# Performance work log

Hardware: AMD Instinct MI355X
Metric: run time of the kernel (lower is better)

## Reference

```python
import jax, jax.numpy as jnp
import numpy as np

H = 128
NUM_IN = 384
B, N, K = 4, 2048, 48
SCALE = 30.0
EPS = 1e-5


def _layernorm(x, gamma, beta):
    mu = jnp.mean(x, axis=-1, keepdims=True)
    var = jnp.mean(jnp.square(x - mu), axis=-1, keepdims=True)
    return (x - mu) * jax.lax.rsqrt(var + EPS) * gamma + beta


def setup_inputs() -> dict:
    key = jax.random.key(0)
    ks = jax.random.split(key, 12)
    s = lambda fan_in: 1.0 / np.sqrt(fan_in)
    inp = {
        "h_V": jax.random.normal(ks[0], (B, N, H), jnp.float32),
        "h_E": jax.random.normal(ks[1], (B, N, K, NUM_IN), jnp.float32),
        "mask_V": jnp.ones((B, N), jnp.float32),
        "mask_attend": jnp.ones((B, N, K), jnp.float32),
        # message MLP
        "W1": jax.random.uniform(ks[2], (H + NUM_IN, H), jnp.float32, -s(H + NUM_IN), s(H + NUM_IN)),
        "b1": jnp.zeros((H,), jnp.float32),
        "W2": jax.random.uniform(ks[3], (H, H), jnp.float32, -s(H), s(H)),
        "b2": jnp.zeros((H,), jnp.float32),
        "W3": jax.random.uniform(ks[4], (H, H), jnp.float32, -s(H), s(H)),
        "b3": jnp.zeros((H,), jnp.float32),
        # layernorms
        "g1": jnp.ones((H,), jnp.float32), "be1": jnp.zeros((H,), jnp.float32),
        "g2": jnp.ones((H,), jnp.float32), "be2": jnp.zeros((H,), jnp.float32),
        # FFN
        "Wi": jax.random.uniform(ks[5], (H, 4 * H), jnp.float32, -s(H), s(H)),
        "bi": jnp.zeros((4 * H,), jnp.float32),
        "Wo": jax.random.uniform(ks[6], (4 * H, H), jnp.float32, -s(4 * H), s(4 * H)),
        "bo": jnp.zeros((H,), jnp.float32),
        # rezero alpha (init 0.01)
        "alpha": jnp.array([0.01], jnp.float32),
    }
    return inp


def reference(h_V, h_E, mask_V, mask_attend, W1, b1, W2, b2, W3, b3,
              g1, be1, g2, be2, Wi, bi, Wo, bo, alpha):
    gelu = lambda x: jax.nn.gelu(x, approximate=False)
    # broadcast-concat node features onto each neighbor edge: [B,N,K,H+num_in]
    h_V_expand = jnp.broadcast_to(h_V[:, :, None, :], (*h_E.shape[:-1], h_V.shape[-1]))
    h_EV = jnp.concatenate([h_V_expand, h_E], axis=-1)
    # 3-layer message MLP
    h_message = gelu(jnp.einsum("bnkf,fh->bnkh", h_EV, W1) + b1)
    h_message = gelu(jnp.einsum("bnkh,hg->bnkg", h_message, W2) + b2)
    h_message = jnp.einsum("bnkg,gh->bnkh", h_message, W3) + b3
    h_message = mask_attend[..., None] * h_message
    # masked sum-reduce over neighbors
    dh = jnp.sum(h_message, axis=-2) / SCALE
    # residual (rezero) + LayerNorm  (dropout = identity in eval)
    h = _layernorm(alpha * dh + h_V, g1, be1)
    # position-wise FFN
    dh = gelu(h @ Wi + bi) @ Wo + bo
    h = _layernorm(alpha * dh + h, g2, be2)
    # node mask
    h = mask_V[..., None] * h
    return h
```

## Files before the change

kernel.cpp:

```cpp
#include <hip/hip_runtime.h>

#define LN_EPS 1e-5f
#define RSCALE (1.0f / 30.0f)

typedef short short8  __attribute__((ext_vector_type(8)));
typedef short short4v __attribute__((ext_vector_type(4)));
typedef float f32x4   __attribute__((ext_vector_type(4)));

__device__ __forceinline__ unsigned short f2bf(float f) {
    unsigned u = __builtin_bit_cast(unsigned, f);
    u = u + 0x7FFFu + ((u >> 16) & 1u);
    return (unsigned short)(u >> 16);
}

__device__ __forceinline__ float gelu_f(float x) {
    float u  = 0.7978845608028654f * (x + 0.044715f * x * x * x);
    float e  = __expf(-2.0f * fabsf(u));
    float t  = 1.0f - 2.0f * e / (1.0f + e);
    return 0.5f * x * (1.0f + copysignf(t, u));
}

__device__ __forceinline__ f32x4 zero4() {
    f32x4 v; v.x = 0.f; v.y = 0.f; v.z = 0.f; v.w = 0.f; return v;
}

__global__ __launch_bounds__(256) void prep_w(
    const float* __restrict__ W1, const float* __restrict__ W2,
    const float* __restrict__ W3,
    unsigned short* __restrict__ w1t, unsigned short* __restrict__ w2t,
    unsigned short* __restrict__ w3t)
{
    int t = blockIdx.x * 256 + threadIdx.x;
    if (t < 65536) {
        int m = t & 127, k = t >> 7;
        w1t[m * 512 + k] = f2bf(W1[k * 128 + m]);
    } else if (t < 81920) {
        int u = t - 65536, m = u & 127, k = u >> 7;
        w2t[m * 128 + k] = f2bf(W2[k * 128 + m]);
    } else if (t < 98304) {
        int u = t - 81920, m = u & 127, k = u >> 7;
        w3t[m * 128 + k] = f2bf(W3[k * 128 + m]);
    }
}

__global__ __launch_bounds__(256, 2) void edge_mlp(
    const float* __restrict__ hV, const float* __restrict__ hE,
    const float* __restrict__ mAtt,
    const unsigned short* __restrict__ w1t, const unsigned short* __restrict__ w2t,
    const unsigned short* __restrict__ w3t,
    const float* __restrict__ b1, const float* __restrict__ b2,
    const float* __restrict__ b3, float* __restrict__ dh)
{
    __shared__ short A1[96 * 64];
    __shared__ short Wb[128 * 64];
    __shared__ short Hb[2][96 * 128];
    __shared__ float mb[96];

    const int tid  = threadIdx.x;
    const int lane = tid & 63;
    const int wv   = tid >> 6;
    const int g    = wv & 1;
    const int mh   = wv >> 1;
    const int ln   = lane & 15;
    const int kg   = lane >> 4;
    const int node0 = blockIdx.x * 2;

    if (tid < 96) mb[tid] = mAtt[node0 * 48 + tid];

    f32x4 acc[4][3];
#pragma unroll
    for (int j = 0; j < 4; ++j)
#pragma unroll
        for (int i = 0; i < 3; ++i) acc[j][i] = zero4();

    const int srow = tid >> 4;
    const int c4   = (tid & 15) * 4;
    const int kb_w = c4 >> 3;
    const int c4lo = c4 & 4;

    for (int c = 0; c < 8; ++c) {
        const int kc = c * 64;
        if (kc < 128) {
#pragma unroll
            for (int rep = 0; rep < 6; ++rep) {
                const int r = rep * 16 + srow;
                const float4 v = *(const float4*)(hV + (node0 + (r >= 48 ? 1 : 0)) * 128 + kc + c4);
                short4v p;
                p.x = (short)f2bf(v.x); p.y = (short)f2bf(v.y);
                p.z = (short)f2bf(v.z); p.w = (short)f2bf(v.w);
                *(short4v*)&A1[r * 64 + ((kb_w ^ (r & 7)) * 8) + c4lo] = p;
            }
        } else {
#pragma unroll
            for (int rep = 0; rep < 6; ++rep) {
                const int r = rep * 16 + srow;
                const float4 v = *(const float4*)(hE + (node0 * 48 + r) * 384 + (kc - 128) + c4);
                short4v p;
                p.x = (short)f2bf(v.x); p.y = (short)f2bf(v.y);
                p.z = (short)f2bf(v.z); p.w = (short)f2bf(v.w);
                *(short4v*)&A1[r * 64 + ((kb_w ^ (r & 7)) * 8) + c4lo] = p;
            }
        }
#pragma unroll
        for (int rep = 0; rep < 4; ++rep) {
            const int u = rep * 256 + tid;
            const int m = u >> 3, kb = u & 7;
            short8 val = *(const short8*)(w1t + m * 512 + kc + kb * 8);
            *(short8*)&Wb[m * 64 + ((kb ^ (m & 7)) * 8)] = val;
        }
        __syncthreads();
#pragma unroll
        for (int s = 0; s < 2; ++s) {
            const int kb = s * 4 + kg;
            short8 bf[3], af[4];
#pragma unroll
            for (int i = 0; i < 3; ++i) {
                const int r = (3 * g + i) * 16 + ln;
                bf[i] = *(const short8*)&A1[r * 64 + ((kb ^ (r & 7)) * 8)];
            }
#pragma unroll
            for (int j = 0; j < 4; ++j) {
                const int m = (4 * mh + j) * 16 + ln;
                af[j] = *(const short8*)&Wb[m * 64 + ((kb ^ (m & 7)) * 8)];
            }
#pragma unroll
            for (int j = 0; j < 4; ++j)
#pragma unroll
                for (int i = 0; i < 3; ++i)
                    acc[j][i] = __builtin_amdgcn_mfma_f32_16x16x32_bf16(af[j], bf[i], acc[j][i], 0, 0, 0);
        }
        __syncthreads();
    }

#pragma unroll
    for (int j = 0; j < 4; ++j) {
        const int m0 = (4 * mh + j) * 16 + kg * 4;
        const float4 bb = *(const float4*)(b1 + m0);
#pragma unroll
        for (int i = 0; i < 3; ++i) {
            const int r = (3 * g + i) * 16 + ln;
            short4v p;
            p.x = (short)f2bf(gelu_f(acc[j][i].x + bb.x));
            p.y = (short)f2bf(gelu_f(acc[j][i].y + bb.y));
            p.z = (short)f2bf(gelu_f(acc[j][i].z + bb.z));
            p.w = (short)f2bf(gelu_f(acc[j][i].w + bb.w));
            *(short4v*)&Hb[0][r * 128 + (((m0 >> 3) ^ (r & 7)) * 8) + (m0 & 4)] = p;
        }
    }

    for (int L = 0; L < 2; ++L) {
#pragma unroll
        for (int j = 0; j < 4; ++j)
#pragma unroll
            for (int i = 0; i < 3; ++i) acc[j][i] = zero4();

        const unsigned short* wt = (L == 0) ? w2t : w3t;
        for (int c = 0; c < 2; ++c) {
            const int kc = c * 64;
#pragma unroll
            for (int rep = 0; rep < 4; ++rep) {
                const int u = rep * 256 + tid;
                const int m = u >> 3, kb = u & 7;
                short8 val = *(const short8*)(wt + m * 128 + kc + kb * 8);
                *(short8*)&Wb[m * 64 + ((kb ^ (m & 7)) * 8)] = val;
            }
            __syncthreads();
#pragma unroll
            for (int s = 0; s < 2; ++s) {
                const int kbW = s * 4 + kg;
                const int kbH = c * 8 + s * 4 + kg;
                short8 bf[3], af[4];
#pragma unroll
                for (int i = 0; i < 3; ++i) {
                    const int r = (3 * g + i) * 16 + ln;
                    bf[i] = *(const short8*)&Hb[L][r * 128 + ((kbH ^ (r & 7)) * 8)];
                }
#pragma unroll
                for (int j = 0; j < 4; ++j) {
                    const int m = (4 * mh + j) * 16 + ln;
                    af[j] = *(const short8*)&Wb[m * 64 + ((kbW ^ (m & 7)) * 8)];
                }
#pragma unroll
                for (int j = 0; j < 4; ++j)
#pragma unroll
                    for (int i = 0; i < 3; ++i)
                        acc[j][i] = __builtin_amdgcn_mfma_f32_16x16x32_bf16(af[j], bf[i], acc[j][i], 0, 0, 0);
            }
            __syncthreads();
        }

        if (L == 0) {
#pragma unroll
            for (int j = 0; j < 4; ++j) {
                const int m0 = (4 * mh + j) * 16 + kg * 4;
                const float4 bb = *(const float4*)(b2 + m0);
#pragma unroll
                for (int i = 0; i < 3; ++i) {
                    const int r = (3 * g + i) * 16 + ln;
                    short4v p;
                    p.x = (short)f2bf(gelu_f(acc[j][i].x + bb.x));
                    p.y = (short)f2bf(gelu_f(acc[j][i].y + bb.y));
                    p.z = (short)f2bf(gelu_f(acc[j][i].z + bb.z));
                    p.w = (short)f2bf(gelu_f(acc[j][i].w + bb.w));
                    *(short4v*)&Hb[1][r * 128 + (((m0 >> 3) ^ (r & 7)) * 8) + (m0 & 4)] = p;
                }
            }
        } else {
#pragma unroll
            for (int j = 0; j < 4; ++j) {
                const int m0 = (4 * mh + j) * 16 + kg * 4;
                const float4 bb = *(const float4*)(b3 + m0);
                float s0 = 0.f, s1 = 0.f, s2 = 0.f, s3 = 0.f;
#pragma unroll
                for (int i = 0; i < 3; ++i) {
                    const int r = (3 * g + i) * 16 + ln;
                    const float mk = mb[r];
                    s0 += (acc[j][i].x + bb.x) * mk;
                    s1 += (acc[j][i].y + bb.y) * mk;
                    s2 += (acc[j][i].z + bb.z) * mk;
                    s3 += (acc[j][i].w + bb.w) * mk;
                }
#pragma unroll
                for (int off = 1; off < 16; off <<= 1) {
                    s0 += __shfl_xor(s0, off, 64);
                    s1 += __shfl_xor(s1, off, 64);
                    s2 += __shfl_xor(s2, off, 64);
                    s3 += __shfl_xor(s3, off, 64);
                }
                if (ln == 0) {
                    float4 o;
                    o.x = s0 * RSCALE; o.y = s1 * RSCALE;
                    o.z = s2 * RSCALE; o.w = s3 * RSCALE;
                    *(float4*)&dh[(node0 + g) * 128 + m0] = o;
                }
            }
        }
    }
}

__global__ __launch_bounds__(256, 2) void node_ffn(
    const float* __restrict__ hV, const float* __restrict__ dh,
    const float* __restrict__ maskV,
    const float* __restrict__ g1, const float* __restrict__ be1,
    const float* __restrict__ g2, const float* __restrict__ be2,
    const float* __restrict__ Wi, const float* __restrict__ bi,
    const float* __restrict__ Wo, const float* __restrict__ bo,
    const float* __restrict__ alphap, float* __restrict__ out)
{
    __shared__ float hbuf[16 * 132];
    __shared__ float hidb[16 * 516];
    __shared__ float obuf[16 * 132];

    const int tid = threadIdx.x;
    const float al = alphap[0];
    const int nb = blockIdx.x * 16;

    {
        const int m = tid >> 4, s = tid & 15;
        const int i0 = s * 8;
        const int base = (nb + m) * 128 + i0;
        float x[8];
        {
            float4 a0 = *(const float4*)(dh + base);
            float4 a1 = *(const float4*)(dh + base + 4);
            float4 v0 = *(const float4*)(hV + base);
            float4 v1 = *(const float4*)(hV + base + 4);
            x[0] = v0.x + al * a0.x; x[1] = v0.y + al * a0.y;
            x[2] = v0.z + al * a0.z; x[3] = v0.w + al * a0.w;
            x[4] = v1.x + al * a1.x; x[5] = v1.y + al * a1.y;
            x[6] = v1.z + al * a1.z; x[7] = v1.w + al * a1.w;
        }
        float sm = 0.f;
#pragma unroll
        for (int q = 0; q < 8; ++q) sm += x[q];
#pragma unroll
        for (int off = 1; off < 16; off <<= 1) sm += __shfl_xor(sm, off, 64);
        const float mu = sm * (1.0f / 128.0f);
        float vs = 0.f;
#pragma unroll
        for (int q = 0; q < 8; ++q) { float d = x[q] - mu; vs += d * d; }
#pragma unroll
        for (int off = 1; off < 16; off <<= 1) vs += __shfl_xor(vs, off, 64);
        const float rs = rsqrtf(vs * (1.0f / 128.0f) + LN_EPS);
#pragma unroll
        for (int q = 0; q < 8; ++q)
            hbuf[m * 132 + i0 + q] = (x[q] - mu) * rs * g1[i0 + q] + be1[i0 + q];
    }
    __syncthreads();

    {
        const int jg = tid & 127, mhh = tid >> 7;
        const int j4 = jg * 4;
        float acc[8][4];
#pragma unroll
        for (int mm = 0; mm < 8; ++mm)
#pragma unroll
            for (int jj = 0; jj < 4; ++jj) acc[mm][jj] = 0.f;
        for (int i0 = 0; i0 < 128; i0 += 4) {
            float4 w0 = *(const float4*)(Wi + (i0 + 0) * 512 + j4);
            float4 w1 = *(const float4*)(Wi + (i0 + 1) * 512 + j4);
            float4 w2 = *(const float4*)(Wi + (i0 + 2) * 512 + j4);
            float4 w3 = *(const float4*)(Wi + (i0 + 3) * 512 + j4);
#pragma unroll
            for (int mm = 0; mm < 8; ++mm) {
                float4 h4 = *(const float4*)&hbuf[(mhh * 8 + mm) * 132 + i0];
                acc[mm][0] += h4.x * w0.x + h4.y * w1.x + h4.z * w2.x + h4.w * w3.x;
                acc[mm][1] += h4.x * w0.y + h4.y * w1.y + h4.z * w2.y + h4.w * w3.y;
                acc[mm][2] += h4.x * w0.z + h4.y * w1.z + h4.z * w2.z + h4.w * w3.z;
                acc[mm][3] += h4.x * w0.w + h4.y * w1.w + h4.z * w2.w + h4.w * w3.w;
            }
        }
        float4 bb = *(const float4*)(bi + j4);
#pragma unroll
        for (int mm = 0; mm < 8; ++mm) {
            float4 o;
            o.x = gelu_f(acc[mm][0] + bb.x);
            o.y = gelu_f(acc[mm][1] + bb.y);
            o.z = gelu_f(acc[mm][2] + bb.z);
            o.w = gelu_f(acc[mm][3] + bb.w);
            *(float4*)&hidb[(mhh * 8 + mm) * 516 + j4] = o;
        }
    }
    __syncthreads();

    {
        const int m = tid >> 4;
        const int n8 = (tid & 15) * 8;
        float4 r0, r1;
        r0.x = r0.y = r0.z = r0.w = 0.f;
        r1.x = r1.y = r1.z = r1.w = 0.f;
        for (int j0 = 0; j0 < 512; j0 += 4) {
            float4 hh = *(const float4*)&hidb[m * 516 + j0];
            float hq[4] = {hh.x, hh.y, hh.z, hh.w};
#pragma unroll
            for (int jj = 0; jj < 4; ++jj) {
                float4 w0 = *(const float4*)(Wo + (j0 + jj) * 128 + n8);
                float4 w1 = *(const float4*)(Wo + (j0 + jj) * 128 + n8 + 4);
                r0.x += hq[jj] * w0.x; r0.y += hq[jj] * w0.y;
                r0.z += hq[jj] * w0.z; r0.w += hq[jj] * w0.w;
                r1.x += hq[jj] * w1.x; r1.y += hq[jj] * w1.y;
                r1.z += hq[jj] * w1.z; r1.w += hq[jj] * w1.w;
            }
        }
        float4 q0 = *(const float4*)(bo + n8);
        float4 q1 = *(const float4*)(bo + n8 + 4);
        r0.x += q0.x; r0.y += q0.y; r0.z += q0.z; r0.w += q0.w;
        r1.x += q1.x; r1.y += q1.y; r1.z += q1.z; r1.w += q1.w;
        *(float4*)&obuf[m * 132 + n8]     = r0;
        *(float4*)&obuf[m * 132 + n8 + 4] = r1;
    }
    __syncthreads();

    {
        const int m = tid >> 4, s = tid & 15;
        const int i0 = s * 8;
        float x[8];
#pragma unroll
        for (int q = 0; q < 8; ++q)
            x[q] = hbuf[m * 132 + i0 + q] + al * obuf[m * 132 + i0 + q];
        float sm = 0.f;
#pragma unroll
        for (int q = 0; q < 8; ++q) sm += x[q];
#pragma unroll
        for (int off = 1; off < 16; off <<= 1) sm += __shfl_xor(sm, off, 64);
        const float mu = sm * (1.0f / 128.0f);
        float vs = 0.f;
#pragma unroll
        for (int q = 0; q < 8; ++q) { float d = x[q] - mu; vs += d * d; }
#pragma unroll
        for (int off = 1; off < 16; off <<= 1) vs += __shfl_xor(vs, off, 64);
        const float rs = rsqrtf(vs * (1.0f / 128.0f) + LN_EPS);
        const float mk = maskV[nb + m];
        float y[8];
#pragma unroll
        for (int q = 0; q < 8; ++q)
            y[q] = ((x[q] - mu) * rs * g2[i0 + q] + be2[i0 + q]) * mk;
        float4 o0, o1;
        o0.x = y[0]; o0.y = y[1]; o0.z = y[2]; o0.w = y[3];
        o1.x = y[4]; o1.y = y[5]; o1.z = y[6]; o1.w = y[7];
        const int base = (nb + m) * 128 + i0;
        *(float4*)(out + base)     = o0;
        *(float4*)(out + base + 4) = o1;
    }
}

extern "C" void kernel_launch(void* const* d_in, const int* in_sizes, int n_in,
                              void* d_out, int out_size, void* d_ws, size_t ws_size,
                              hipStream_t stream)
{
    const float* hV  = (const float*)d_in[0];
    const float* hE  = (const float*)d_in[1];
    const float* mV  = (const float*)d_in[2];
    const float* mA  = (const float*)d_in[3];
    const float* W1  = (const float*)d_in[4];
    const float* b1  = (const float*)d_in[5];
    const float* W2  = (const float*)d_in[6];
    const float* b2  = (const float*)d_in[7];
    const float* W3  = (const float*)d_in[8];
    const float* b3  = (const float*)d_in[9];
    const float* g1  = (const float*)d_in[10];
    const float* be1 = (const float*)d_in[11];
    const float* g2  = (const float*)d_in[12];
    const float* be2 = (const float*)d_in[13];
    const float* Wi  = (const float*)d_in[14];
    const float* bi  = (const float*)d_in[15];
    const float* Wo  = (const float*)d_in[16];
    const float* bo  = (const float*)d_in[17];
    const float* al  = (const float*)d_in[18];
    float* out = (float*)d_out;

    float* dh = (float*)d_ws;
    unsigned short* w1t = (unsigned short*)((char*)d_ws + (size_t)4194304);
    unsigned short* w2t = w1t + 65536;
    unsigned short* w3t = w2t + 16384;

    prep_w  <<<384,  256, 0, stream>>>(W1, W2, W3, w1t, w2t, w3t);
    edge_mlp<<<4096, 256, 0, stream>>>(hV, hE, mA, w1t, w2t, w3t, b1, b2, b3, dh);
    node_ffn<<<512,  256, 0, stream>>>(hV, dh, mV, g1, be1, g2, be2, Wi, bi, Wo, bo, al, out);
}
```

Baseline: 989.0 us.

## Precompute per-node h_V projection once and drop node K-chunks from edge GEMM

The node part of the first layer (h_V · W1[:128]) is the same for all 48 neighbours, so it is now computed once per node in fp32 and used to seed the MFMA accumulators, together with b1. The edge GEMM's K loop shrinks from 8 chunks to 6. This cuts redundant MFMA work and repeated h_V loads and conversions. The second hidden buffer is dropped so LDS use falls, and launch bounds rise to 3 blocks per CU for more occupancy. The cost is a small scalar fp32 dot product per block that reads W1 columns with stride, though these should stay in cache.

```diff
diff --git a/kernel.cpp b/kernel.cpp
--- a/kernel.cpp
+++ b/kernel.cpp
@@ -27,33 +27,34 @@
 __global__ __launch_bounds__(256) void prep_w(
     const float* __restrict__ W1, const float* __restrict__ W2,
     const float* __restrict__ W3,
-    unsigned short* __restrict__ w1t, unsigned short* __restrict__ w2t,
+    unsigned short* __restrict__ w1bt, unsigned short* __restrict__ w2t,
     unsigned short* __restrict__ w3t)
 {
     int t = blockIdx.x * 256 + threadIdx.x;
-    if (t < 65536) {
-        int m = t & 127, k = t >> 7;
-        w1t[m * 512 + k] = f2bf(W1[k * 128 + m]);
+    if (t < 49152) {
+        int m = t & 127, kk = t >> 7;
+        w1bt[m * 384 + kk] = f2bf(W1[(kk + 128) * 128 + m]);
+    } else if (t < 65536) {
+        int u = t - 49152, m = u & 127, k = u >> 7;
+        w2t[m * 128 + k] = f2bf(W2[k * 128 + m]);
     } else if (t < 81920) {
         int u = t - 65536, m = u & 127, k = u >> 7;
-        w2t[m * 128 + k] = f2bf(W2[k * 128 + m]);
-    } else if (t < 98304) {
-        int u = t - 81920, m = u & 127, k = u >> 7;
         w3t[m * 128 + k] = f2bf(W3[k * 128 + m]);
     }
 }
 
-__global__ __launch_bounds__(256, 2) void edge_mlp(
+__global__ __launch_bounds__(256, 3) void edge_mlp(
     const float* __restrict__ hV, const float* __restrict__ hE,
     const float* __restrict__ mAtt,
-    const unsigned short* __restrict__ w1t, const unsigned short* __restrict__ w2t,
+    const float* __restrict__ W1, const float* __restrict__ b1,
+    const unsigned short* __restrict__ w1bt, const unsigned short* __restrict__ w2t,
     const unsigned short* __restrict__ w3t,
-    const float* __restrict__ b1, const float* __restrict__ b2,
-    const float* __restrict__ b3, float* __restrict__ dh)
+    const float* __restrict__ b2, const float* __restrict__ b3,
+    float* __restrict__ dh)
 {
-    __shared__ short A1[96 * 64];
-    __shared__ short Wb[128 * 64];
-    __shared__ short Hb[2][96 * 128];
+    __shared__ __align__(16) short A1[96 * 64];
+    __shared__ __align__(16) short Wb[128 * 64];
+    __shared__ __align__(16) short Hb[96 * 128];
     __shared__ float mb[96];
 
     const int tid  = threadIdx.x;
@@ -65,47 +66,58 @@
     const int kg   = lane >> 4;
     const int node0 = blockIdx.x * 2;
 
-    if (tid < 96) mb[tid] = mAtt[node0 * 48 + tid];
-
-    f32x4 acc[4][3];
-#pragma unroll
-    for (int j = 0; j < 4; ++j)
-#pragma unroll
-        for (int i = 0; i < 3; ++i) acc[j][i] = zero4();
-
     const int srow = tid >> 4;
     const int c4   = (tid & 15) * 4;
     const int kb_w = c4 >> 3;
     const int c4lo = c4 & 4;
 
-    for (int c = 0; c < 8; ++c) {
+    if (tid < 96) mb[tid] = mAtt[node0 * 48 + tid];
+
+    float* nv = (float*)A1;
+    {
+        const int gg = tid >> 7, m = tid & 127;
+        const float* hv = hV + (node0 + gg) * 128;
+        const float* wc = W1 + m;
+        float a0 = 0.f, a1 = 0.f, a2 = 0.f, a3 = 0.f;
+        for (int k = 0; k < 128; k += 4) {
+            const float4 h4 = *(const float4*)(hv + k);
+            a0 += h4.x * wc[(k + 0) * 128];
+            a1 += h4.y * wc[(k + 1) * 128];
+            a2 += h4.z * wc[(k + 2) * 128];
+            a3 += h4.w * wc[(k + 3) * 128];
+        }
+        nv[tid] = b1[m] + (a0 + a1) + (a2 + a3);
+    }
+    __syncthreads();
+
+    f32x4 acc[4][3];
+#pragma unroll
+    for (int j = 0; j < 4; ++j) {
+        const float4 iv = *(const float4*)&nv[g * 128 + (4 * mh + j) * 16 + kg * 4];
+#pragma unroll
+        for (int i = 0; i < 3; ++i) {
+            acc[j][i].x = iv.x; acc[j][i].y = iv.y;
+            acc[j][i].z = iv.z; acc[j][i].w = iv.w;
+        }
+    }
+    __syncthreads();
+
+    for (int c = 0; c < 6; ++c) {
         const int kc = c * 64;
-        if (kc < 128) {
-#pragma unroll
-            for (int rep = 0; rep < 6; ++rep) {
-                const int r = rep * 16 + srow;
-                const float4 v = *(const float4*)(hV + (node0 + (r >= 48 ? 1 : 0)) * 128 + kc + c4);
-                short4v p;
-                p.x = (short)f2bf(v.x); p.y = (short)f2bf(v.y);
-                p.z = (short)f2bf(v.z); p.w = (short)f2bf(v.w);
-                *(short4v*)&A1[r * 64 + ((kb_w ^ (r & 7)) * 8) + c4lo] = p;
-            }
-        } else {
-#pragma unroll
-            for (int rep = 0; rep < 6; ++rep) {
-                const int r = rep * 16 + srow;
-                const float4 v = *(const float4*)(hE + (node0 * 48 + r) * 384 + (kc - 128) + c4);
-                short4v p;
-                p.x = (short)f2bf(v.x); p.y = (short)f2bf(v.y);
-                p.z = (short)f2bf(v.z); p.w = (short)f2bf(v.w);
-                *(short4v*)&A1[r * 64 + ((kb_w ^ (r & 7)) * 8) + c4lo] = p;
-            }
+#pragma unroll
+        for (int rep = 0; rep < 6; ++rep) {
+            const int r = rep * 16 + srow;
+            const float4 v = *(const float4*)(hE + (node0 * 48 + r) * 384 + kc + c4);
+            short4v p;
+            p.x = (short)f2bf(v.x); p.y = (short)f2bf(v.y);
+            p.z = (short)f2bf(v.z); p.w = (short)f2bf(v.w);
+            *(short4v*)&A1[r * 64 + ((kb_w ^ (r & 7)) * 8) + c4lo] = p;
         }
 #pragma unroll
         for (int rep = 0; rep < 4; ++rep) {
             const int u = rep * 256 + tid;
             const int m = u >> 3, kb = u & 7;
-            short8 val = *(const short8*)(w1t + m * 512 + kc + kb * 8);
+            short8 val = *(const short8*)(w1bt + m * 384 + kc + kb * 8);
             *(short8*)&Wb[m * 64 + ((kb ^ (m & 7)) * 8)] = val;
         }
         __syncthreads();
@@ -135,16 +147,15 @@
 #pragma unroll
     for (int j = 0; j < 4; ++j) {
         const int m0 = (4 * mh + j) * 16 + kg * 4;
-        const float4 bb = *(const float4*)(b1 + m0);
 #pragma unroll
         for (int i = 0; i < 3; ++i) {
             const int r = (3 * g + i) * 16 + ln;
             short4v p;
-            p.x = (short)f2bf(gelu_f(acc[j][i].x + bb.x));
-            p.y = (short)f2bf(gelu_f(acc[j][i].y + bb.y));
-            p.z = (short)f2bf(gelu_f(acc[j][i].z + bb.z));
-            p.w = (short)f2bf(gelu_f(acc[j][i].w + bb.w));
-            *(short4v*)&Hb[0][r * 128 + (((m0 >> 3) ^ (r & 7)) * 8) + (m0 & 4)] = p;
+            p.x = (short)f2bf(gelu_f(acc[j][i].x));
+            p.y = (short)f2bf(gelu_f(acc[j][i].y));
+            p.z = (short)f2bf(gelu_f(acc[j][i].z));
+            p.w = (short)f2bf(gelu_f(acc[j][i].w));
+            *(short4v*)&Hb[r * 128 + (((m0 >> 3) ^ (r & 7)) * 8) + (m0 & 4)] = p;
         }
     }
 
@@ -173,7 +184,7 @@
 #pragma unroll
                 for (int i = 0; i < 3; ++i) {
                     const int r = (3 * g + i) * 16 + ln;
-                    bf[i] = *(const short8*)&Hb[L][r * 128 + ((kbH ^ (r & 7)) * 8)];
+                    bf[i] = *(const short8*)&Hb[r * 128 + ((kbH ^ (r & 7)) * 8)];
                 }
 #pragma unroll
                 for (int j = 0; j < 4; ++j) {
@@ -202,7 +213,7 @@
                     p.y = (short)f2bf(gelu_f(acc[j][i].y + bb.y));
                     p.z = (short)f2bf(gelu_f(acc[j][i].z + bb.z));
                     p.w = (short)f2bf(gelu_f(acc[j][i].w + bb.w));
-                    *(short4v*)&Hb[1][r * 128 + (((m0 >> 3) ^ (r & 7)) * 8) + (m0 & 4)] = p;
+                    *(short4v*)&Hb[r * 128 + (((m0 >> 3) ^ (r & 7)) * 8) + (m0 & 4)] = p;
                 }
             }
         } else {
@@ -410,11 +421,11 @@
     float* out = (float*)d_out;
 
     float* dh = (float*)d_ws;
-    unsigned short* w1t = (unsigned short*)((char*)d_ws + (size_t)4194304);
-    unsigned short* w2t = w1t + 65536;
+    unsigned short* w1bt = (unsigned short*)((char*)d_ws + (size_t)4194304);
+    unsigned short* w2t = w1bt + 49152;
     unsigned short* w3t = w2t + 16384;
 
-    prep_w  <<<384,  256, 0, stream>>>(W1, W2, W3, w1t, w2t, w3t);
-    edge_mlp<<<4096, 256, 0, stream>>>(hV, hE, mA, w1t, w2t, w3t, b1, b2, b3, dh);
+    prep_w  <<<320,  256, 0, stream>>>(W1, W2, W3, w1bt, w2t, w3t);
+    edge_mlp<<<4096, 256, 0, stream>>>(hV, hE, mA, W1, b1, w1bt, w2t, w3t, b2, b3, dh);
     node_ffn<<<512,  256, 0, stream>>>(hV, dh, mV, g1, be1, g2, be2, Wi, bi, Wo, bo, al, out);
 }
```

Result: faster. 938.7 us (-5.1%).
